# Kernel optimization log

Hardware: AMD Instinct MI355X
Metric: run time of the kernel (lower is better)

The kernel has to match this reference:

```python
import jax, jax.numpy as jnp
import numpy as np

B, T, D, H = 4, 1024, 1024, 16
HD = D // H
DFF = 2048          # ExpertTier hidden width
K = 3               # ConvTier causal kernel size
NEG = -1e9


def layernorm(x, w, b, eps=1e-5):
    m = jnp.mean(x, axis=-1, keepdims=True)
    v = jnp.var(x, axis=-1, keepdims=True)
    return (x - m) * jax.lax.rsqrt(v + eps) * w + b


def rope_cos_sin(t, hd):
    inv = 1.0 / (10000.0 ** (jnp.arange(0, hd, 2, dtype=jnp.float32) / hd))
    freqs = jnp.outer(jnp.arange(t, dtype=jnp.float32), inv)  # (T, hd/2)
    return jnp.cos(freqs), jnp.sin(freqs)


def apply_rope(x, cos, sin):
    # x: (B, H, T, hd); cos/sin: (T, hd/2)
    x1, x2 = jnp.split(x, 2, axis=-1)
    return jnp.concatenate([x1 * cos - x2 * sin, x1 * sin + x2 * cos], axis=-1)


def causal_attn(q, k, v):
    # q,k,v: (..., T, d); full causal softmax attention
    t = q.shape[-2]
    scale = 1.0 / jnp.sqrt(jnp.asarray(q.shape[-1], q.dtype))
    scores = jnp.einsum('...qd,...kd->...qk', q, k) * scale
    mask = jnp.triu(jnp.ones((t, t), dtype=bool), k=1)
    scores = jnp.where(mask, NEG, scores)
    w = jax.nn.softmax(scores, axis=-1)
    return jnp.einsum('...qk,...kd->...qd', w, v)


def setup_inputs() -> dict:
    key = jax.random.key(0)
    ks = jax.random.split(key, 16)
    ws = 0.02
    g = lambda k, shape, s: jax.random.normal(k, shape, dtype=jnp.float32) * s
    return {
        'x': g(ks[0], (B, T, D), 1.0),
        'ln1_w': jnp.ones((D,), jnp.float32), 'ln1_b': jnp.zeros((D,), jnp.float32),
        'qkv_w': g(ks[1], (D, 3 * D), ws),
        'out_w': g(ks[2], (D, D), ws),
        'ln2_w': jnp.ones((D,), jnp.float32), 'ln2_b': jnp.zeros((D,), jnp.float32),
        'router_w': g(ks[3], (D, 4), ws),
        'conv_w': g(ks[4], (D, 1, K), 0.1),             # depthwise OIW, groups=D
        'expert_w1': g(ks[5], (D, DFF), ws),
        'expert_w2': g(ks[6], (DFF, D), ws),
        'at_wq': g(ks[7], (D, D), ws),
        'at_wk': g(ks[8], (D, D), ws),
        'at_wv': g(ks[9], (D, D), ws),
        'at_wo': g(ks[10], (D, D), ws),
        'tier_gate': jnp.full((D,), 0.1, jnp.float32),
        'sink_kv_scale': jnp.asarray(0.1, jnp.float32),
    }


def reference(x, ln1_w, ln1_b, qkv_w, out_w, ln2_w, ln2_b, router_w, conv_w,
              expert_w1, expert_w2, at_wq, at_wk, at_wv, at_wo,
              tier_gate, sink_kv_scale):
    b, t, d = x.shape
    # --- backbone causal self-attention with RoPE (pre-norm) ---
    h1 = layernorm(x, ln1_w, ln1_b)
    qkv = (h1 @ qkv_w).reshape(b, t, 3, H, HD)
    q = qkv[:, :, 0].transpose(0, 2, 1, 3)  # (B,H,T,hd)
    k = qkv[:, :, 1].transpose(0, 2, 1, 3)
    v = qkv[:, :, 2].transpose(0, 2, 1, 3)
    cos, sin = rope_cos_sin(t, HD)
    q = apply_rope(q, cos, sin)
    k = apply_rope(k, cos, sin)
    ao = causal_attn(q, k, v)                         # (B,H,T,hd)
    ao = ao.transpose(0, 2, 1, 3).reshape(b, t, d) @ out_w
    x = x + ao
    # --- router + tiers ---
    h = layernorm(x, ln2_w, ln2_b)
    routing_w = jax.nn.softmax(h @ router_w, axis=-1)  # (B,T,4): conv/expert/attn/sink
    # ConvTier: depthwise causal conv (k=3) + GELU
    hc = jnp.pad(h.transpose(0, 2, 1), ((0, 0), (0, 0), (K - 1, 0)))  # (B,D,T+K-1)
    conv = jax.lax.conv_general_dilated(hc, conv_w, (1,), 'VALID',
                                        feature_group_count=d,
                                        dimension_numbers=('NCH', 'OIH', 'NCH'))
    conv_out = jax.nn.gelu(conv.transpose(0, 2, 1))   # (B,T,D)
    # ExpertTier: 2-layer GELU MLP
    expert_out = jax.nn.gelu(h @ expert_w1) @ expert_w2
    # AttentionTier: single-head causal attention
    attn2 = causal_attn(h @ at_wq, h @ at_wk, h @ at_wv) @ at_wo
    # SinkTier outputs zeros -> contributes nothing to the weighted sum
    combined = (conv_out * routing_w[..., 0:1]
                + expert_out * routing_w[..., 1:2]
                + attn2 * routing_w[..., 2:3])
    x = x + combined * tier_gate
    # sink kv scaling
    kv_scale = 1.0 - routing_w[..., 3] * (1.0 - jnp.abs(sink_kv_scale))
    x = x * kv_scale[..., None]
    return (x, routing_w)
```

## Files before the change

### kernel.cpp

```cpp
#include <hip/hip_runtime.h>

#define Bz 4
#define Tz 1024
#define Dz 1024
#define Hz 16
#define NTz (Bz*Tz)

typedef short s8v __attribute__((ext_vector_type(8)));
typedef float f4v __attribute__((ext_vector_type(4)));

__device__ __forceinline__ float bf2f(unsigned short u){
  unsigned int x = ((unsigned int)u) << 16;
  return __builtin_bit_cast(float, x);
}
__device__ __forceinline__ unsigned short f2bf(float f){
  unsigned int x = __builtin_bit_cast(unsigned int, f);
  x += 0x7fffu + ((x >> 16) & 1u);
  return (unsigned short)(x >> 16);
}
__device__ __forceinline__ float gelu_f(float x){
  float z = 1.5957691216057308f * (x + 0.044715f * x * x * x);
  return x / (1.0f + __expf(-z));
}
__device__ __forceinline__ void gl16(const unsigned short* g, unsigned short* l){
  __builtin_amdgcn_global_load_lds(
      (const __attribute__((address_space(1))) unsigned int*)g,
      (__attribute__((address_space(3))) unsigned int*)l, 16, 0, 0);
}

__global__ __launch_bounds__(256) void k_convtrans(const float* __restrict__ in,
    unsigned short* __restrict__ out, int R, int C)
{
  __shared__ float tile[32][33];
  int c0 = blockIdx.x * 32, r0 = blockIdx.y * 32;
  int tx = threadIdx.x & 31, ty = threadIdx.x >> 5;
  #pragma unroll
  for (int i = 0; i < 32; i += 8)
    tile[ty + i][tx] = in[(long)(r0 + ty + i) * C + c0 + tx];
  __syncthreads();
  #pragma unroll
  for (int i = 0; i < 32; i += 8)
    out[(long)(c0 + ty + i) * R + r0 + tx] = f2bf(tile[tx][ty + i]);
}

__global__ __launch_bounds__(256) void k_convtrans_b(const unsigned short* __restrict__ in,
    unsigned short* __restrict__ out, int ld, long sIn, long sOut)
{
  __shared__ unsigned short tile[32][34];
  in  += (long)blockIdx.z * sIn;
  out += (long)blockIdx.z * sOut;
  int c0 = blockIdx.x * 32, r0 = blockIdx.y * 32;
  int tx = threadIdx.x & 31, ty = threadIdx.x >> 5;
  #pragma unroll
  for (int i = 0; i < 32; i += 8)
    tile[ty + i][tx] = in[(long)(r0 + ty + i) * ld + c0 + tx];
  __syncthreads();
  #pragma unroll
  for (int i = 0; i < 32; i += 8)
    out[(long)(c0 + ty + i) * 1024 + r0 + tx] = tile[tx][ty + i];
}

__global__ __launch_bounds__(256) void k_layernorm(const float* __restrict__ x,
    const float* __restrict__ w, const float* __restrict__ b,
    unsigned short* __restrict__ out)
{
  int row = blockIdx.x, tid = threadIdx.x;
  const float4* xp = (const float4*)(x + (long)row * Dz);
  float4 v = xp[tid];
  float s  = v.x + v.y + v.z + v.w;
  float ss = v.x*v.x + v.y*v.y + v.z*v.z + v.w*v.w;
  int lane = tid & 63, wv = tid >> 6;
  #pragma unroll
  for (int off = 32; off; off >>= 1){ s += __shfl_xor(s, off); ss += __shfl_xor(ss, off); }
  __shared__ float red[8];
  if (lane == 0){ red[wv] = s; red[4 + wv] = ss; }
  __syncthreads();
  s  = red[0] + red[1] + red[2] + red[3];
  ss = red[4] + red[5] + red[6] + red[7];
  float mean = s * (1.0f / Dz);
  float var  = ss * (1.0f / Dz) - mean * mean;
  float rstd = rsqrtf(var + 1e-5f);
  float4 wg = ((const float4*)w)[tid];
  float4 bg = ((const float4*)b)[tid];
  ushort4 ov;
  ov.x = f2bf((v.x - mean) * rstd * wg.x + bg.x);
  ov.y = f2bf((v.y - mean) * rstd * wg.y + bg.y);
  ov.z = f2bf((v.z - mean) * rstd * wg.z + bg.z);
  ov.w = f2bf((v.w - mean) * rstd * wg.w + bg.w);
  *((ushort4*)(out + (long)row * Dz) + tid) = ov;
}

__global__ __launch_bounds__(256) void k_ln_router(const float* __restrict__ x,
    const float* __restrict__ w, const float* __restrict__ b,
    const float* __restrict__ rw, unsigned short* __restrict__ out,
    float* __restrict__ rout)
{
  int row = blockIdx.x, tid = threadIdx.x;
  const float4* xp = (const float4*)(x + (long)row * Dz);
  float4 v = xp[tid];
  float s  = v.x + v.y + v.z + v.w;
  float ss = v.x*v.x + v.y*v.y + v.z*v.z + v.w*v.w;
  int lane = tid & 63, wv = tid >> 6;
  #pragma unroll
  for (int off = 32; off; off >>= 1){ s += __shfl_xor(s, off); ss += __shfl_xor(ss, off); }
  __shared__ float red[8];
  if (lane == 0){ red[wv] = s; red[4 + wv] = ss; }
  __syncthreads();
  s  = red[0] + red[1] + red[2] + red[3];
  ss = red[4] + red[5] + red[6] + red[7];
  float mean = s * (1.0f / Dz);
  float var  = ss * (1.0f / Dz) - mean * mean;
  float rstd = rsqrtf(var + 1e-5f);
  float4 wg = ((const float4*)w)[tid];
  float4 bg = ((const float4*)b)[tid];
  float h0 = (v.x - mean) * rstd * wg.x + bg.x;
  float h1 = (v.y - mean) * rstd * wg.y + bg.y;
  float h2 = (v.z - mean) * rstd * wg.z + bg.z;
  float h3 = (v.w - mean) * rstd * wg.w + bg.w;
  ushort4 ov;
  ov.x = f2bf(h0); ov.y = f2bf(h1); ov.z = f2bf(h2); ov.w = f2bf(h3);
  *((ushort4*)(out + (long)row * Dz) + tid) = ov;
  int d0 = tid * 4;
  float4 r0 = *(const float4*)(rw + (long)d0 * 4);
  float4 r1 = *(const float4*)(rw + (long)(d0 + 1) * 4);
  float4 r2 = *(const float4*)(rw + (long)(d0 + 2) * 4);
  float4 r3 = *(const float4*)(rw + (long)(d0 + 3) * 4);
  float a0 = h0*r0.x + h1*r1.x + h2*r2.x + h3*r3.x;
  float a1 = h0*r0.y + h1*r1.y + h2*r2.y + h3*r3.y;
  float a2 = h0*r0.z + h1*r1.z + h2*r2.z + h3*r3.z;
  float a3 = h0*r0.w + h1*r1.w + h2*r2.w + h3*r3.w;
  #pragma unroll
  for (int off = 32; off; off >>= 1) {
    a0 += __shfl_xor(a0, off); a1 += __shfl_xor(a1, off);
    a2 += __shfl_xor(a2, off); a3 += __shfl_xor(a3, off);
  }
  __shared__ float red2[4][4];
  if (lane == 0){ red2[wv][0] = a0; red2[wv][1] = a1; red2[wv][2] = a2; red2[wv][3] = a3; }
  __syncthreads();
  if (tid == 0) {
    float s0 = red2[0][0] + red2[1][0] + red2[2][0] + red2[3][0];
    float s1 = red2[0][1] + red2[1][1] + red2[2][1] + red2[3][1];
    float s2 = red2[0][2] + red2[1][2] + red2[2][2] + red2[3][2];
    float s3 = red2[0][3] + red2[1][3] + red2[2][3] + red2[3][3];
    float mx = fmaxf(fmaxf(s0, s1), fmaxf(s2, s3));
    float e0 = __expf(s0 - mx), e1 = __expf(s1 - mx);
    float e2 = __expf(s2 - mx), e3 = __expf(s3 - mx);
    float inv = 1.0f / (e0 + e1 + e2 + e3);
    float4 r = {e0 * inv, e1 * inv, e2 * inv, e3 * inv};
    *(float4*)(rout + (long)row * 4) = r;
  }
}

template<int MODE, int BN, bool TRIMAP, bool TRIK, bool DBUF>
__global__ __launch_bounds__(256) void k_gemm(
    const unsigned short* __restrict__ A,
    const unsigned short* __restrict__ Bt,
    float* __restrict__ Cf, unsigned short* __restrict__ Cb,
    const float* __restrict__ addsrc,
    unsigned short* __restrict__ P1, unsigned short* __restrict__ P2,
    int N, int K, int lda, int ldb,
    long sA, long sB, long sC)
{
  constexpr int BM = 128;
  constexpr int MREP = (BN == 128) ? 4 : 2;
  constexpr int NB = DBUF ? 2 : 1;
  __shared__ unsigned short As[NB][BM * 64];
  __shared__ unsigned short Bs[NB][BN * 64];
  int bm, bn;
  if (TRIMAP) {
    int li = blockIdx.x;
    int nwg = gridDim.x;
    if ((nwg & 7) == 0) li = (li & 7) * (nwg >> 3) + (li >> 3);
    int r = (int)((sqrtf(4.f * li + 1.f) - 1.f) * 0.5f);
    if ((r + 1) * (r + 2) <= li) ++r;
    if (r * (r + 1) > li) --r;
    bm = r * 128; bn = (li - r * (r + 1)) * BN;
  } else {
    int lin = blockIdx.y * gridDim.x + blockIdx.x;
    int nwg = gridDim.x * gridDim.y;
    if ((nwg & 7) == 0) lin = (lin & 7) * (nwg >> 3) + (lin >> 3);
    int cols = gridDim.x, rows = gridDim.y;
    constexpr int GM = 8;
    int in_grp = GM * cols;
    int gid = lin / in_grp;
    int fm = gid * GM;
    int gsz = min(rows - fm, GM);
    int rem = lin - gid * in_grp;
    int pm = fm + (rem % gsz);
    int pn = rem / gsz;
    if (TRIK) pm = rows - 1 - pm;
    bm = pm * BM; bn = pn * BN;
  }
  A  += (long)blockIdx.z * sA;
  Bt += (long)blockIdx.z * sB;
  int tid = threadIdx.x, w = tid >> 6, lane = tid & 63;
  int wr, wc;
  if (BN == 128) { wr = (w >> 1) * 64; wc = (w & 1) * 64; }
  else           { wr = w * 32;        wc = 0; }
  f4v acc[MREP][4];
  #pragma unroll
  for (int m = 0; m < MREP; ++m)
    #pragma unroll
    for (int n = 0; n < 4; ++n)
      acc[m][n] = (f4v){0.f, 0.f, 0.f, 0.f};

  int Keff = K;
  if (TRIK) Keff = min(K, bm + BM);

  int lrow = lane >> 3;
  int lcol = (((lane & 7) ^ lrow) * 8);
  const unsigned short* AgJ[4];
  int AsOff[4];
  #pragma unroll
  for (int j = 0; j < 4; ++j) {
    AgJ[j] = A + (long)(bm + w * 32 + j * 8 + lrow) * lda + lcol;
    AsOff[j] = (w * 32 + j * 8) * 64;
  }
  constexpr int BCH = BN / 8 / 4;
  const unsigned short* BgJ[BCH];
  int BsOff[BCH];
  #pragma unroll
  for (int j = 0; j < BCH; ++j) {
    BgJ[j] = Bt + (long)(bn + w * (BCH * 8) + j * 8 + lrow) * ldb + lcol;
    BsOff[j] = (w * (BCH * 8) + j * 8) * 64;
  }

  int fr = lane & 15, fg = lane >> 4;
  int sw = (fr & 7) * 8;

  auto stage = [&](int buf, int k0){
    #pragma unroll
    for (int j = 0; j < 4; ++j) gl16(AgJ[j] + k0, &As[buf][AsOff[j]]);
    #pragma unroll
    for (int j = 0; j < BCH; ++j) gl16(BgJ[j] + k0, &Bs[buf][BsOff[j]]);
  };
  auto compute = [&](int buf){
    #pragma unroll
    for (int kk = 0; kk < 2; ++kk) {
      int kg = (kk * 32 + fg * 8) ^ sw;
      s8v af[MREP], bfv[4];
      #pragma unroll
      for (int m = 0; m < MREP; ++m) af[m]  = *(const s8v*)&As[buf][(wr + m * 16 + fr) * 64 + kg];
      #pragma unroll
      for (int n = 0; n < 4; ++n)    bfv[n] = *(const s8v*)&Bs[buf][(wc + n * 16 + fr) * 64 + kg];
      #pragma unroll
      for (int m = 0; m < MREP; ++m)
        #pragma unroll
        for (int n = 0; n < 4; ++n)
          acc[m][n] = __builtin_amdgcn_mfma_f32_16x16x32_bf16(af[m], bfv[n], acc[m][n], 0, 0, 0);
    }
  };

  if (DBUF) {
    int cur = 0;
    stage(0, 0);
    __syncthreads();
    for (int k0 = 0; k0 < Keff; k0 += 64) {
      if (k0 + 64 < Keff) stage(cur ^ 1, k0 + 64);
      compute(cur);
      __syncthreads();
      cur ^= 1;
    }
  } else {
    for (int k0 = 0; k0 < Keff; k0 += 64) {
      __syncthreads();
      stage(0, k0);
      __syncthreads();
      compute(0);
    }
  }

  int cr0 = bm + wr + fg * 4;
  int cc0 = bn + wc + fr;

  if (MODE == 4) {
    int sect = bn >> 10;
    if (sect == 2) {
      #pragma unroll
      for (int m = 0; m < MREP; ++m)
        #pragma unroll
        for (int n = 0; n < 4; ++n)
          #pragma unroll
          for (int i = 0; i < 4; ++i) {
            int row = cr0 + m * 16 + i;
            int vcol = (bn - 2048) + wc + n * 16 + fr;
            P2[(long)row * 1024 + vcol] = f2bf(acc[m][n][i]);
          }
    } else {
      unsigned short* dst = (sect == 0) ? Cb : P1;
      float scl = (sect == 0) ? 0.125f : 1.0f;
      int head = ((bn & 1023) + wc) >> 6;
      float inv0 = exp2f(-(float)fr * 0.4152410118609203f);
      float inv1 = exp2f(-(float)(fr + 16) * 0.4152410118609203f);
      #pragma unroll
      for (int m = 0; m < MREP; ++m)
        #pragma unroll
        for (int i = 0; i < 4; ++i) {
          int row = cr0 + m * 16 + i;
          int t = row & 1023, bq = row >> 10;
          float a0 = (float)t * inv0, a1 = (float)t * inv1;
          float cs0 = __cosf(a0), sn0 = __sinf(a0);
          float cs1 = __cosf(a1), sn1 = __sinf(a1);
          float v0 = acc[m][0][i], v1 = acc[m][1][i];
          float v2 = acc[m][2][i], v3 = acc[m][3][i];
          long base = ((long)(bq * 16 + head)) * 65536 + (long)t * 64 + fr;
          dst[base]      = f2bf((v0 * cs0 - v2 * sn0) * scl);
          dst[base + 32] = f2bf((v0 * sn0 + v2 * cs0) * scl);
          dst[base + 16] = f2bf((v1 * cs1 - v3 * sn1) * scl);
          dst[base + 48] = f2bf((v1 * sn1 + v3 * cs1) * scl);
        }
    }
    return;
  }

  #pragma unroll
  for (int m = 0; m < MREP; ++m)
    #pragma unroll
    for (int n = 0; n < 4; ++n)
      #pragma unroll
      for (int i = 0; i < 4; ++i) {
        long row = cr0 + m * 16 + i, col = cc0 + n * 16;
        long idx = (long)blockIdx.z * sC + row * (long)N + col;
        float v = acc[m][n][i];
        if (MODE == 1) v += addsrc[idx];
        if (MODE == 5) { if (col < 2048) v = gelu_f(v); }
        if (MODE == 6) v *= 0.03125f;
        if (MODE <= 1) Cf[idx] = v; else Cb[idx] = f2bf(v);
      }
}

__global__ __launch_bounds__(256) void k_attn_mfma(
    const unsigned short* __restrict__ Qb, const unsigned short* __restrict__ Kb,
    const unsigned short* __restrict__ Vt, unsigned short* __restrict__ ao)
{
  __shared__ unsigned short Ks[64][72];
  __shared__ unsigned short Vs[64][72];
  __shared__ unsigned short Ps[4][16][72];
  int qb = 15 - (blockIdx.x >> 6);
  int bh = blockIdx.x & 63;
  int b = bh >> 4, h = bh & 15;
  int t0 = qb * 64;
  int tid = threadIdx.x, w = tid >> 6, lane = tid & 63;
  int fr = lane & 15, fg = lane >> 4;

  const unsigned short* qp = Qb + (long)bh * Tz * 64 + (long)(t0 + w * 16 + fr) * 64 + fg * 8;
  s8v qf[2] = { *(const s8v*)qp, *(const s8v*)(qp + 32) };

  f4v o_acc[4];
  #pragma unroll
  for (int n = 0; n < 4; ++n) o_acc[n] = (f4v){0.f, 0.f, 0.f, 0.f};
  float m_[4] = {-1e30f, -1e30f, -1e30f, -1e30f};
  float l_[4] = {0.f, 0.f, 0.f, 0.f};

  int sr = tid >> 3, sc = (tid & 7) * 8;
  const unsigned short* Kg = Kb + (long)bh * Tz * 64 + (long)sr * 64 + sc;
  const unsigned short* Vg = Vt + (long)bh * 64 * Tz + (long)sr * Tz + sc;

  for (int kt = 0; kt <= qb; ++kt) {
    int k0 = kt * 64;
    __syncthreads();
    *(uint4*)&Ks[sr][sc]      = *(const uint4*)(Kg + (long)k0 * 64);
    *(uint4*)&Ks[sr + 32][sc] = *(const uint4*)(Kg + (long)(k0 + 32) * 64);
    *(uint4*)&Vs[sr][sc]      = *(const uint4*)(Vg + k0);
    *(uint4*)&Vs[sr + 32][sc] = *(const uint4*)(Vg + (long)32 * Tz + k0);
    __syncthreads();

    f4v sacc[4];
    #pragma unroll
    for (int n = 0; n < 4; ++n) sacc[n] = (f4v){0.f, 0.f, 0.f, 0.f};
    #pragma unroll
    for (int kk = 0; kk < 2; ++kk) {
      int kg = kk * 32 + fg * 8;
      #pragma unroll
      for (int n = 0; n < 4; ++n) {
        s8v bf = *(const s8v*)&Ks[n * 16 + fr][kg];
        sacc[n] = __builtin_amdgcn_mfma_f32_16x16x32_bf16(qf[kk], bf, sacc[n], 0, 0, 0);
      }
    }

    bool full = (kt < qb);
    float p[4][4], alpha[4];
    #pragma unroll
    for (int i = 0; i < 4; ++i) {
      int trow = t0 + w * 16 + fg * 4 + i;
      float mx = -1e30f;
      #pragma unroll
      for (int n = 0; n < 4; ++n) {
        float sval = sacc[n][i];
        if (!full) {
          int key = k0 + n * 16 + fr;
          sval = (key <= trow) ? sval : -1e30f;
        }
        p[n][i] = sval;
        mx = fmaxf(mx, sval);
      }
      mx = fmaxf(mx, __shfl_xor(mx, 1));
      mx = fmaxf(mx, __shfl_xor(mx, 2));
      mx = fmaxf(mx, __shfl_xor(mx, 4));
      mx = fmaxf(mx, __shfl_xor(mx, 8));
      float mnew = fmaxf(m_[i], mx);
      alpha[i] = __expf(m_[i] - mnew);
      m_[i] = mnew;
      float ps = 0.f;
      #pragma unroll
      for (int n = 0; n < 4; ++n) {
        float pv = __expf(p[n][i] - mnew);
        p[n][i] = pv;
        ps += pv;
      }
      ps += __shfl_xor(ps, 1); ps += __shfl_xor(ps, 2);
      ps += __shfl_xor(ps, 4); ps += __shfl_xor(ps, 8);
      l_[i] = l_[i] * alpha[i] + ps;
    }
    #pragma unroll
    for (int n = 0; n < 4; ++n)
      #pragma unroll
      for (int i = 0; i < 4; ++i)
        o_acc[n][i] *= alpha[i];
    #pragma unroll
    for (int n = 0; n < 4; ++n)
      #pragma unroll
      for (int i = 0; i < 4; ++i)
        Ps[w][fg * 4 + i][n * 16 + fr] = f2bf(p[n][i]);

    #pragma unroll
    for (int kk = 0; kk < 2; ++kk) {
      int kg = kk * 32 + fg * 8;
      s8v pa = *(const s8v*)&Ps[w][fr][kg];
      #pragma unroll
      for (int n = 0; n < 4; ++n) {
        s8v vb = *(const s8v*)&Vs[n * 16 + fr][kg];
        o_acc[n] = __builtin_amdgcn_mfma_f32_16x16x32_bf16(pa, vb, o_acc[n], 0, 0, 0);
      }
    }
  }

  float inv[4];
  #pragma unroll
  for (int i = 0; i < 4; ++i) inv[i] = 1.0f / l_[i];
  #pragma unroll
  for (int n = 0; n < 4; ++n)
    #pragma unroll
    for (int i = 0; i < 4; ++i) {
      int t = t0 + w * 16 + fg * 4 + i;
      ao[((long)(b * Tz + t)) * Dz + h * 64 + n * 16 + fr] = f2bf(o_acc[n][i] * inv[i]);
    }
}

__global__ __launch_bounds__(256) void k_softmax_causal(const unsigned short* __restrict__ S,
    unsigned short* __restrict__ P)
{
  long row = blockIdx.x;
  int t = (int)(row & (Tz - 1));
  int tid = threadIdx.x;
  const unsigned short* sp = S + row * Tz;
  ushort4 v = ((const ushort4*)sp)[tid];
  float vv[4];
  vv[0] = (tid*4 + 0 <= t) ? bf2f(v.x) : -1e30f;
  vv[1] = (tid*4 + 1 <= t) ? bf2f(v.y) : -1e30f;
  vv[2] = (tid*4 + 2 <= t) ? bf2f(v.z) : -1e30f;
  vv[3] = (tid*4 + 3 <= t) ? bf2f(v.w) : -1e30f;
  float mx = fmaxf(fmaxf(vv[0], vv[1]), fmaxf(vv[2], vv[3]));
  int lane = tid & 63, wv = tid >> 6;
  #pragma unroll
  for (int off = 32; off; off >>= 1) mx = fmaxf(mx, __shfl_xor(mx, off));
  __shared__ float red[8];
  if (lane == 0) red[wv] = mx;
  __syncthreads();
  mx = fmaxf(fmaxf(red[0], red[1]), fmaxf(red[2], red[3]));
  float p[4];
  float s = 0.f;
  #pragma unroll
  for (int i = 0; i < 4; ++i){ p[i] = __expf(vv[i] - mx); s += p[i]; }
  #pragma unroll
  for (int off = 32; off; off >>= 1) s += __shfl_xor(s, off);
  if (lane == 0) red[4 + wv] = s;
  __syncthreads();
  s = red[4] + red[5] + red[6] + red[7];
  float inv = 1.0f / s;
  ushort4 ov;
  ov.x = f2bf(p[0] * inv); ov.y = f2bf(p[1] * inv);
  ov.z = f2bf(p[2] * inv); ov.w = f2bf(p[3] * inv);
  *((ushort4*)(P + row * Tz) + tid) = ov;
}

__global__ __launch_bounds__(256) void k_combine(
    const float* __restrict__ x2, const unsigned short* __restrict__ hbf,
    const unsigned short* __restrict__ eo, const unsigned short* __restrict__ ap,
    const float* __restrict__ rout, const float* __restrict__ convw,
    const float* __restrict__ tg, const float* __restrict__ sinkp,
    float* __restrict__ outx)
{
  int row = blockIdx.x, tid = threadIdx.x;
  int t = row & (Tz - 1), b = row >> 10;
  int d0 = tid * 4;
  float4 x4 = *(const float4*)(x2 + (long)row * Dz + d0);
  ushort4 e4 = *(const ushort4*)(eo + (long)row * Dz + d0);
  ushort4 a4 = *(const ushort4*)(ap + (long)row * Dz + d0);
  float4 t4 = *(const float4*)(tg + d0);
  float4 r4 = *(const float4*)(rout + (long)row * 4);
  float sks = fabsf(sinkp[0]);
  float kv = 1.0f - r4.w * (1.0f - sks);
  const float4* cwp = (const float4*)(convw + (long)d0 * 3);
  float4 c0 = cwp[0], c1 = cwp[1], c2 = cwp[2];
  float cwf[12] = {c0.x, c0.y, c0.z, c0.w, c1.x, c1.y, c1.z, c1.w, c2.x, c2.y, c2.z, c2.w};
  float hv[3][4];
  #pragma unroll
  for (int tap = 0; tap < 3; ++tap) {
    int tt = t - 2 + tap;
    if (tt >= 0) {
      ushort4 hu = *((const ushort4*)(hbf + ((long)(b * Tz + tt)) * Dz + d0));
      hv[tap][0] = bf2f(hu.x); hv[tap][1] = bf2f(hu.y);
      hv[tap][2] = bf2f(hu.z); hv[tap][3] = bf2f(hu.w);
    } else {
      hv[tap][0] = 0.f; hv[tap][1] = 0.f; hv[tap][2] = 0.f; hv[tap][3] = 0.f;
    }
  }
  float ov[4];
  float xi[4] = {x4.x, x4.y, x4.z, x4.w};
  float ei[4] = {bf2f(e4.x), bf2f(e4.y), bf2f(e4.z), bf2f(e4.w)};
  float ai[4] = {bf2f(a4.x), bf2f(a4.y), bf2f(a4.z), bf2f(a4.w)};
  float ti[4] = {t4.x, t4.y, t4.z, t4.w};
  #pragma unroll
  for (int i = 0; i < 4; ++i) {
    float conv = hv[0][i] * cwf[i*3 + 0] + hv[1][i] * cwf[i*3 + 1] + hv[2][i] * cwf[i*3 + 2];
    float comb = gelu_f(conv) * r4.x + ei[i] * r4.y + ai[i] * r4.z;
    ov[i] = (xi[i] + comb * ti[i]) * kv;
  }
  float4 res = {ov[0], ov[1], ov[2], ov[3]};
  *(float4*)(outx + (long)row * Dz + d0) = res;
}

extern "C" void kernel_launch(void* const* d_in, const int* in_sizes, int n_in,
                              void* d_out, int out_size, void* d_ws, size_t ws_size,
                              hipStream_t stream) {
  (void)in_sizes; (void)n_in; (void)out_size; (void)ws_size;
  const float* x       = (const float*)d_in[0];
  const float* ln1_w   = (const float*)d_in[1];
  const float* ln1_b   = (const float*)d_in[2];
  const float* qkv_w   = (const float*)d_in[3];
  const float* out_w   = (const float*)d_in[4];
  const float* ln2_w   = (const float*)d_in[5];
  const float* ln2_b   = (const float*)d_in[6];
  const float* router_w= (const float*)d_in[7];
  const float* conv_w  = (const float*)d_in[8];
  const float* ew1     = (const float*)d_in[9];
  const float* ew2     = (const float*)d_in[10];
  const float* at_wq   = (const float*)d_in[11];
  const float* at_wk   = (const float*)d_in[12];
  const float* at_wv   = (const float*)d_in[13];
  const float* at_wo   = (const float*)d_in[14];
  const float* tg      = (const float*)d_in[15];
  const float* sinkp   = (const float*)d_in[16];
  float* outx = (float*)d_out;
  float* rout = outx + (size_t)NTz * Dz;

  char* ws = (char*)d_ws;
  size_t off = 0;
  auto alloc = [&](size_t bytes) -> char* {
    char* p = ws + off;
    off += (bytes + 255) & ~(size_t)255;
    return p;
  };
  const long TD = (long)Tz * Dz, TT = (long)Tz * Tz;

  unsigned short* w_qkvt  = (unsigned short*)alloc((size_t)3072*1024*2);
  unsigned short* w_outt  = (unsigned short*)alloc((size_t)1024*1024*2);
  unsigned short* w_tiert = (unsigned short*)alloc((size_t)5120*1024*2);
  unsigned short* w_ew2t  = (unsigned short*)alloc((size_t)1024*2048*2);
  unsigned short* w_wot   = (unsigned short*)alloc((size_t)1024*1024*2);
  unsigned short* h1bf    = (unsigned short*)alloc((size_t)NTz*Dz*2);
  unsigned short* tierb   = (unsigned short*)alloc((size_t)NTz*5120*2);
  unsigned short* aobf    = (unsigned short*)alloc((size_t)NTz*Dz*2);
  float*          x2f     = (float*)alloc((size_t)NTz*Dz*4);
  unsigned short* hbf     = (unsigned short*)alloc((size_t)NTz*Dz*2);
  unsigned short* Pbf     = (unsigned short*)alloc((size_t)Bz*Tz*Tz*2);
  unsigned short* v2tbf   = (unsigned short*)alloc((size_t)NTz*Dz*2);
  unsigned short* a2obf   = (unsigned short*)alloc((size_t)NTz*Dz*2);
  unsigned short* eofb    = (unsigned short*)alloc((size_t)NTz*Dz*2);
  unsigned short* a2pb    = (unsigned short*)alloc((size_t)NTz*Dz*2);
  unsigned short* Sbf     = (unsigned short*)alloc((size_t)Bz*Tz*Tz*2);

  unsigned short* Qb = (unsigned short*)x2f;
  unsigned short* Kb = Pbf;
  unsigned short* Vb = tierb;
  unsigned short* Vt = a2pb;

  dim3 blk(256);

  k_convtrans<<<dim3(96, 32), blk, 0, stream>>>(qkv_w, w_qkvt, 1024, 3072);
  k_convtrans<<<dim3(32, 32), blk, 0, stream>>>(out_w, w_outt, 1024, 1024);
  k_convtrans<<<dim3(64, 32), blk, 0, stream>>>(ew1,   w_tiert,                 1024, 2048);
  k_convtrans<<<dim3(32, 32), blk, 0, stream>>>(at_wq, w_tiert + 2048*1024,     1024, 1024);
  k_convtrans<<<dim3(32, 32), blk, 0, stream>>>(at_wk, w_tiert + 3072*1024,     1024, 1024);
  k_convtrans<<<dim3(32, 32), blk, 0, stream>>>(at_wv, w_tiert + (size_t)4096*1024, 1024, 1024);
  k_convtrans<<<dim3(32, 64), blk, 0, stream>>>(ew2,   w_ew2t, 2048, 1024);
  k_convtrans<<<dim3(32, 32), blk, 0, stream>>>(at_wo, w_wot, 1024, 1024);

  k_layernorm<<<NTz, blk, 0, stream>>>(x, ln1_w, ln1_b, h1bf);
  k_gemm<4,128,false,false,false><<<dim3(24, 32), blk, 0, stream>>>(h1bf, w_qkvt,
      nullptr, Qb, nullptr, Kb, Vb, 3072, 1024, 1024, 1024, 0, 0, 0);
  k_convtrans_b<<<dim3(32, 32, 4), blk, 0, stream>>>(Vb, Vt, 1024, TD, TD);
  k_attn_mfma<<<dim3(1024), blk, 0, stream>>>(Qb, Kb, Vt, aobf);
  k_gemm<1,64,false,false,true><<<dim3(16, 32), blk, 0, stream>>>(aobf, w_outt, x2f,
      nullptr, x, nullptr, nullptr, 1024, 1024, 1024, 1024, 0, 0, 0);
  k_ln_router<<<NTz, blk, 0, stream>>>(x2f, ln2_w, ln2_b, router_w, hbf, rout);
  k_gemm<5,128,false,false,false><<<dim3(40, 32), blk, 0, stream>>>(hbf, w_tiert,
      nullptr, tierb, nullptr, nullptr, nullptr, 5120, 1024, 1024, 1024, 0, 0, 0);
  k_gemm<3,64,false,false,true><<<dim3(16, 32), blk, 0, stream>>>(tierb, w_ew2t, nullptr,
      eofb, nullptr, nullptr, nullptr, 1024, 2048, 5120, 2048, 0, 0, 0);
  k_convtrans_b<<<dim3(32, 32, 4), blk, 0, stream>>>(tierb + 4096, v2tbf, 5120,
      (long)Tz*5120, TD);
  k_gemm<6,64,true,false,true><<<dim3(72, 1, 4), blk, 0, stream>>>(tierb + 2048,
      tierb + 3072, nullptr, Sbf, nullptr, nullptr, nullptr,
      1024, 1024, 5120, 5120, (long)Tz*5120, (long)Tz*5120, TT);
  k_softmax_causal<<<NTz, blk, 0, stream>>>(Sbf, Pbf);
  k_gemm<3,64,false,true,true><<<dim3(16, 8, 4), blk, 0, stream>>>(Pbf, v2tbf, nullptr,
      a2obf, nullptr, nullptr, nullptr, 1024, 1024, 1024, 1024, TT, TD, TD);
  k_gemm<3,64,false,false,true><<<dim3(16, 32), blk, 0, stream>>>(a2obf, w_wot, nullptr,
      a2pb, nullptr, nullptr, nullptr, 1024, 1024, 1024, 1024, 0, 0, 0);
  k_combine<<<NTz, blk, 0, stream>>>(x2f, hbf, eofb, a2pb, rout, conv_w, tg, sinkp, outx);
}
```

Baseline: 306.2 us.

## Batch weight transposes, prefetch attention tiles, split-K expert GEMM, flip GEMM flags

The eight per-weight transpose launches become one packed launch that uses a segment table. The flash-attention loop now prefetches the next K/V tile into registers while the current tile is being computed. The second expert GEMM is split along K into two batched halves whose partial outputs are summed in the combine kernel, which gives more blocks to a grid that was small. Two GEMM instantiations also have a template flag changed, likely selecting a different kernel variant. Together these add register pressure, an extra partial-output buffer and read in the combine kernel, and a precision change from summing two bf16 partials.

```diff
diff --git a/kernel.cpp b/kernel.cpp
--- a/kernel.cpp
+++ b/kernel.cpp
@@ -28,11 +28,23 @@
       (__attribute__((address_space(3))) unsigned int*)l, 16, 0, 0);
 }
 
-__global__ __launch_bounds__(256) void k_convtrans(const float* __restrict__ in,
-    unsigned short* __restrict__ out, int R, int C)
+struct WSeg { const float* in; unsigned short* out; int R, C, blk0, bx; };
+struct WPack { WSeg s[8]; };
+__global__ __launch_bounds__(256) void k_convtrans_all(WPack p)
 {
   __shared__ float tile[32][33];
-  int c0 = blockIdx.x * 32, r0 = blockIdx.y * 32;
+  int bid = blockIdx.x;
+  const float* in = p.s[0].in; unsigned short* out = p.s[0].out;
+  int R = p.s[0].R, C = p.s[0].C, blk0 = 0, bx = p.s[0].bx;
+  #pragma unroll
+  for (int i = 1; i < 8; ++i) {
+    if (bid >= p.s[i].blk0) {
+      in = p.s[i].in; out = p.s[i].out; R = p.s[i].R; C = p.s[i].C;
+      blk0 = p.s[i].blk0; bx = p.s[i].bx;
+    }
+  }
+  int rel = bid - blk0;
+  int c0 = (rel % bx) * 32, r0 = (rel / bx) * 32;
   int tx = threadIdx.x & 31, ty = threadIdx.x >> 5;
   #pragma unroll
   for (int i = 0; i < 32; i += 8)
@@ -356,14 +368,27 @@
   const unsigned short* Kg = Kb + (long)bh * Tz * 64 + (long)sr * 64 + sc;
   const unsigned short* Vg = Vt + (long)bh * 64 * Tz + (long)sr * Tz + sc;
 
+  uint4 pk0, pk1, pv0, pv1;
+  auto loadregs = [&](int k0){
+    pk0 = *(const uint4*)(Kg + (long)k0 * 64);
+    pk1 = *(const uint4*)(Kg + (long)(k0 + 32) * 64);
+    pv0 = *(const uint4*)(Vg + k0);
+    pv1 = *(const uint4*)(Vg + (long)32 * Tz + k0);
+  };
+  auto storelds = [&](){
+    *(uint4*)&Ks[sr][sc]      = pk0;
+    *(uint4*)&Ks[sr + 32][sc] = pk1;
+    *(uint4*)&Vs[sr][sc]      = pv0;
+    *(uint4*)&Vs[sr + 32][sc] = pv1;
+  };
+
+  loadregs(0);
+  storelds();
+  __syncthreads();
+
   for (int kt = 0; kt <= qb; ++kt) {
     int k0 = kt * 64;
-    __syncthreads();
-    *(uint4*)&Ks[sr][sc]      = *(const uint4*)(Kg + (long)k0 * 64);
-    *(uint4*)&Ks[sr + 32][sc] = *(const uint4*)(Kg + (long)(k0 + 32) * 64);
-    *(uint4*)&Vs[sr][sc]      = *(const uint4*)(Vg + k0);
-    *(uint4*)&Vs[sr + 32][sc] = *(const uint4*)(Vg + (long)32 * Tz + k0);
-    __syncthreads();
+    if (kt < qb) loadregs(k0 + 64);
 
     f4v sacc[4];
     #pragma unroll
@@ -433,6 +458,12 @@
         o_acc[n] = __builtin_amdgcn_mfma_f32_16x16x32_bf16(pa, vb, o_acc[n], 0, 0, 0);
       }
     }
+
+    if (kt < qb) {
+      __syncthreads();
+      storelds();
+      __syncthreads();
+    }
   }
 
   float inv[4];
@@ -486,7 +517,8 @@
 
 __global__ __launch_bounds__(256) void k_combine(
     const float* __restrict__ x2, const unsigned short* __restrict__ hbf,
-    const unsigned short* __restrict__ eo, const unsigned short* __restrict__ ap,
+    const unsigned short* __restrict__ eoa, const unsigned short* __restrict__ eob,
+    const unsigned short* __restrict__ ap,
     const float* __restrict__ rout, const float* __restrict__ convw,
     const float* __restrict__ tg, const float* __restrict__ sinkp,
     float* __restrict__ outx)
@@ -495,7 +527,8 @@
   int t = row & (Tz - 1), b = row >> 10;
   int d0 = tid * 4;
   float4 x4 = *(const float4*)(x2 + (long)row * Dz + d0);
-  ushort4 e4 = *(const ushort4*)(eo + (long)row * Dz + d0);
+  ushort4 ea = *(const ushort4*)(eoa + (long)row * Dz + d0);
+  ushort4 eb = *(const ushort4*)(eob + (long)row * Dz + d0);
   ushort4 a4 = *(const ushort4*)(ap + (long)row * Dz + d0);
   float4 t4 = *(const float4*)(tg + d0);
   float4 r4 = *(const float4*)(rout + (long)row * 4);
@@ -518,7 +551,8 @@
   }
   float ov[4];
   float xi[4] = {x4.x, x4.y, x4.z, x4.w};
-  float ei[4] = {bf2f(e4.x), bf2f(e4.y), bf2f(e4.z), bf2f(e4.w)};
+  float ei[4] = {bf2f(ea.x) + bf2f(eb.x), bf2f(ea.y) + bf2f(eb.y),
+                 bf2f(ea.z) + bf2f(eb.z), bf2f(ea.w) + bf2f(eb.w)};
   float ai[4] = {bf2f(a4.x), bf2f(a4.y), bf2f(a4.z), bf2f(a4.w)};
   float ti[4] = {t4.x, t4.y, t4.z, t4.w};
   #pragma unroll
@@ -585,30 +619,35 @@
   unsigned short* Kb = Pbf;
   unsigned short* Vb = tierb;
   unsigned short* Vt = a2pb;
+  unsigned short* eofb2 = h1bf;
+  long eoDelta = (long)(eofb2 - eofb);
 
   dim3 blk(256);
 
-  k_convtrans<<<dim3(96, 32), blk, 0, stream>>>(qkv_w, w_qkvt, 1024, 3072);
-  k_convtrans<<<dim3(32, 32), blk, 0, stream>>>(out_w, w_outt, 1024, 1024);
-  k_convtrans<<<dim3(64, 32), blk, 0, stream>>>(ew1,   w_tiert,                 1024, 2048);
-  k_convtrans<<<dim3(32, 32), blk, 0, stream>>>(at_wq, w_tiert + 2048*1024,     1024, 1024);
-  k_convtrans<<<dim3(32, 32), blk, 0, stream>>>(at_wk, w_tiert + 3072*1024,     1024, 1024);
-  k_convtrans<<<dim3(32, 32), blk, 0, stream>>>(at_wv, w_tiert + (size_t)4096*1024, 1024, 1024);
-  k_convtrans<<<dim3(32, 64), blk, 0, stream>>>(ew2,   w_ew2t, 2048, 1024);
-  k_convtrans<<<dim3(32, 32), blk, 0, stream>>>(at_wo, w_wot, 1024, 1024);
+  WPack wp;
+  wp.s[0] = {qkv_w, w_qkvt,                         1024, 3072, 0,     96};
+  wp.s[1] = {out_w, w_outt,                         1024, 1024, 3072,  32};
+  wp.s[2] = {ew1,   w_tiert,                        1024, 2048, 4096,  64};
+  wp.s[3] = {at_wq, w_tiert + 2048*1024,            1024, 1024, 6144,  32};
+  wp.s[4] = {at_wk, w_tiert + 3072*1024,            1024, 1024, 7168,  32};
+  wp.s[5] = {at_wv, w_tiert + (size_t)4096*1024,    1024, 1024, 8192,  32};
+  wp.s[6] = {ew2,   w_ew2t,                         2048, 1024, 9216,  32};
+  wp.s[7] = {at_wo, w_wot,                          1024, 1024, 11264, 32};
+  k_convtrans_all<<<dim3(12288), blk, 0, stream>>>(wp);
 
   k_layernorm<<<NTz, blk, 0, stream>>>(x, ln1_w, ln1_b, h1bf);
-  k_gemm<4,128,false,false,false><<<dim3(24, 32), blk, 0, stream>>>(h1bf, w_qkvt,
+  k_gemm<4,128,false,false,true><<<dim3(24, 32), blk, 0, stream>>>(h1bf, w_qkvt,
       nullptr, Qb, nullptr, Kb, Vb, 3072, 1024, 1024, 1024, 0, 0, 0);
   k_convtrans_b<<<dim3(32, 32, 4), blk, 0, stream>>>(Vb, Vt, 1024, TD, TD);
   k_attn_mfma<<<dim3(1024), blk, 0, stream>>>(Qb, Kb, Vt, aobf);
   k_gemm<1,64,false,false,true><<<dim3(16, 32), blk, 0, stream>>>(aobf, w_outt, x2f,
       nullptr, x, nullptr, nullptr, 1024, 1024, 1024, 1024, 0, 0, 0);
   k_ln_router<<<NTz, blk, 0, stream>>>(x2f, ln2_w, ln2_b, router_w, hbf, rout);
-  k_gemm<5,128,false,false,false><<<dim3(40, 32), blk, 0, stream>>>(hbf, w_tiert,
+  k_gemm<5,128,false,false,true><<<dim3(40, 32), blk, 0, stream>>>(hbf, w_tiert,
       nullptr, tierb, nullptr, nullptr, nullptr, 5120, 1024, 1024, 1024, 0, 0, 0);
-  k_gemm<3,64,false,false,true><<<dim3(16, 32), blk, 0, stream>>>(tierb, w_ew2t, nullptr,
-      eofb, nullptr, nullptr, nullptr, 1024, 2048, 5120, 2048, 0, 0, 0);
+  k_gemm<3,64,false,false,true><<<dim3(16, 32, 2), blk, 0, stream>>>(tierb, w_ew2t,
+      nullptr, eofb, nullptr, nullptr, nullptr, 1024, 1024, 5120, 2048,
+      1024, 1024, eoDelta);
   k_convtrans_b<<<dim3(32, 32, 4), blk, 0, stream>>>(tierb + 4096, v2tbf, 5120,
       (long)Tz*5120, TD);
   k_gemm<6,64,true,false,true><<<dim3(72, 1, 4), blk, 0, stream>>>(tierb + 2048,
@@ -619,5 +658,6 @@
       a2obf, nullptr, nullptr, nullptr, 1024, 1024, 1024, 1024, TT, TD, TD);
   k_gemm<3,64,false,false,true><<<dim3(16, 32), blk, 0, stream>>>(a2obf, w_wot, nullptr,
       a2pb, nullptr, nullptr, nullptr, 1024, 1024, 1024, 1024, 0, 0, 0);
-  k_combine<<<NTz, blk, 0, stream>>>(x2f, hbf, eofb, a2pb, rout, conv_w, tg, sinkp, outx);
-}
+  k_combine<<<NTz, blk, 0, stream>>>(x2f, hbf, eofb, eofb2, a2pb, rout, conv_w,
+      tg, sinkp, outx);
+}
```

New measurement: 302.1 us. About the same (-1.3%).
